# Kernel optimization log

Measured on AMD Instinct MI355X. Metric: run time of the kernel, lower is better.

Reference implementation:

```python
import jax, jax.numpy as jnp
import numpy as np

NUM_BINS = 4
NUM_CELLS = NUM_BINS ** 3


def _generate_grids(num_bins):
    # cell-center coordinates in the unit cube, matching generate_grids()
    c = (jnp.arange(num_bins, dtype=jnp.float32) + 1.0) / num_bins - 0.5 / num_bins
    gx, gy, gz = jnp.meshgrid(c, c, c, indexing='ij')
    return jnp.stack([gx.ravel(), gy.ravel(), gz.ravel()], axis=1)  # [C, 3]


def setup_inputs() -> dict:
    key = jax.random.key(0)
    x = jax.random.normal(key, (64, 65536, 6), dtype=jnp.float32)
    return {"input": x}


def reference(input):
    B, P, _ = input.shape
    pos = input[..., 0:3]
    ori = input[..., 3:6]

    # symmetric bounding cube: bbox_max over points and xyz dims
    bbox_max = jnp.max(jnp.abs(pos), axis=(1, 2), keepdims=True)          # [B,1,1]
    thickness = jnp.clip(2.0 * bbox_max, 1e-5, None)
    pos_in_cube = (pos + bbox_max) / thickness                            # [B,P,3] in [0,1]

    ci = jnp.clip((pos_in_cube * NUM_BINS).astype(jnp.int32), 0, NUM_BINS - 1)
    cell_idx = (ci[..., 0] * NUM_BINS + ci[..., 1]) * NUM_BINS + ci[..., 2]  # [B,P]

    seg = lambda vals, idx: jax.ops.segment_sum(vals, idx, num_segments=NUM_CELLS)

    # per-cell point counts
    freq = jax.vmap(seg)(jnp.ones((B, P), jnp.float32), cell_idx)[..., None]  # [B,C,1]
    freq_c = jnp.clip(freq, 1.0, None)
    uprefix = 1.0 / jnp.sqrt(freq_c)
    f_freq = 0.001 * freq * uprefix                                       # [B,C,1]

    # mean offset from cell centers
    grids = _generate_grids(NUM_BINS)                                     # [C,3]
    offsets = pos_in_cube - grids[cell_idx]                               # [B,P,3]
    f_mean = jax.vmap(seg)(offsets, cell_idx) * uprefix                   # [B,C,3]

    # upper-triangular orientation covariance: xx,xy,xz,yy,yz,zz
    ox, oy, oz = ori[..., 0], ori[..., 1], ori[..., 2]
    cov = jnp.stack([ox * ox, ox * oy, ox * oz, oy * oy, oy * oz, oz * oz], axis=-1)  # [B,P,6]
    f_normcov = jax.vmap(seg)(cov, cell_idx) / freq_c                     # [B,C,6]

    f_all = jnp.concatenate([f_freq, f_mean, f_normcov], axis=2).reshape(B, -1)  # [B, C*10]
    norm = jnp.linalg.norm(f_all, axis=1, keepdims=True)
    return f_all / jnp.clip(norm, 1e-12, None)
```

## Files before the change

kernel.cpp:

```cpp
#include <hip/hip_runtime.h>


#define BATCH 64
#define NPTS 65536
#define FEAT 640
#define COPIES 16
#define CSTRIDE 16
#define S_OFF 262144.0f
#define S_COV 4096.0f

__device__ __forceinline__ void bin_point(int* h, int k,
                                          float px, float py, float pz,
                                          float ox, float oy, float oz,
                                          float bmax, float inv_thick) {
    float sx = (px + bmax) * inv_thick;
    float sy = (py + bmax) * inv_thick;
    float sz = (pz + bmax) * inv_thick;
    int cx = (int)(sx * 4.0f); cx = cx < 0 ? 0 : (cx > 3 ? 3 : cx);
    int cy = (int)(sy * 4.0f); cy = cy < 0 ? 0 : (cy > 3 ? 3 : cy);
    int cz = (int)(sz * 4.0f); cz = cz < 0 ? 0 : (cz > 3 ? 3 : cz);
    int cell = (cx * 4 + cy) * 4 + cz;
    float offx = sx - (cx * 0.25f + 0.125f);
    float offy = sy - (cy * 0.25f + 0.125f);
    float offz = sz - (cz * 0.25f + 0.125f);
    int kk = k ^ (cell & 15);
    int a = cell * (10 * CSTRIDE) + kk;
    atomicAdd(&h[a + 0 * CSTRIDE], 1);
    atomicAdd(&h[a + 1 * CSTRIDE], __float2int_rn(offx * S_OFF));
    atomicAdd(&h[a + 2 * CSTRIDE], __float2int_rn(offy * S_OFF));
    atomicAdd(&h[a + 3 * CSTRIDE], __float2int_rn(offz * S_OFF));
    atomicAdd(&h[a + 4 * CSTRIDE], __float2int_rn(ox * ox * S_COV));
    atomicAdd(&h[a + 5 * CSTRIDE], __float2int_rn(ox * oy * S_COV));
    atomicAdd(&h[a + 6 * CSTRIDE], __float2int_rn(ox * oz * S_COV));
    atomicAdd(&h[a + 7 * CSTRIDE], __float2int_rn(oy * oy * S_COV));
    atomicAdd(&h[a + 8 * CSTRIDE], __float2int_rn(oy * oz * S_COV));
    atomicAdd(&h[a + 9 * CSTRIDE], __float2int_rn(oz * oz * S_COV));
}

__global__ __launch_bounds__(256) void k_bbox(const float* __restrict__ x,
                                              unsigned int* __restrict__ part,
                                              unsigned long long* __restrict__ acc) {
    int b = blockIdx.y;
    int fb = b * 16 + blockIdx.x;
    if (threadIdx.x < 40) acc[fb * 40 + threadIdx.x] = 0ULL;

    const float4* F = (const float4*)(x + (size_t)b * NPTS * 6);
    int tid = blockIdx.x * 256 + threadIdx.x;
    int tm = tid % 3;
    float m = 0.0f;
    #pragma unroll
    for (int o = 0; o < 2; ++o) {
        #pragma unroll
        for (int u = 0; u < 12; ++u) {
            int it = o * 12 + u;
            float4 v = F[tid + it * 4096];
            int mm = tm + (u % 3);
            mm = mm >= 3 ? mm - 3 : mm;
            float ax = fabsf(v.x), ay = fabsf(v.y), az = fabsf(v.z), aw = fabsf(v.w);
            float c0 = fmaxf(fmaxf(ax, ay), az);
            float c1 = fmaxf(az, aw);
            float cand = mm == 0 ? c0 : (mm == 1 ? c1 : ax);
            m = fmaxf(m, cand);
        }
    }
    for (int off = 32; off > 0; off >>= 1) m = fmaxf(m, __shfl_down(m, off, 64));
    __shared__ float s[4];
    if ((threadIdx.x & 63) == 0) s[threadIdx.x >> 6] = m;
    __syncthreads();
    if (threadIdx.x == 0) {
        m = fmaxf(fmaxf(s[0], s[1]), fmaxf(s[2], s[3]));
        part[fb] = __float_as_uint(m);
    }
}

__global__ __launch_bounds__(256) void k_bin(const float* __restrict__ x,
                                             const unsigned int* __restrict__ part,
                                             unsigned long long* __restrict__ acc) {
    __shared__ int h[FEAT * CSTRIDE];
    for (int i = threadIdx.x; i < FEAT * CSTRIDE; i += 256) h[i] = 0;
    int b = blockIdx.y;
    unsigned int um = 0u;
    #pragma unroll
    for (int p = 0; p < 16; ++p) um = um > part[b * 16 + p] ? um : part[b * 16 + p];
    float bmax = __uint_as_float(um);
    float thick = fmaxf(2.0f * bmax, 1e-5f);
    float inv_thick = 1.0f / thick;
    __syncthreads();

    const float4* base = (const float4*)(x + (size_t)b * NPTS * 6);
    int tid = blockIdx.x * 256 + threadIdx.x;
    int k = threadIdx.x & (COPIES - 1);
    #pragma unroll
    for (int it = 0; it < 8; ++it) {
        int i = tid + it * 4096;
        float4 f0 = base[3 * i + 0];
        float4 f1 = base[3 * i + 1];
        float4 f2 = base[3 * i + 2];
        bin_point(h, k, f0.x, f0.y, f0.z, f0.w, f1.x, f1.y, bmax, inv_thick);
        bin_point(h, k, f1.z, f1.w, f2.x, f2.y, f2.z, f2.w, bmax, inv_thick);
    }
    __syncthreads();
    for (int v = threadIdx.x; v < FEAT; v += 256) {
        long long sum = 0;
        #pragma unroll
        for (int c = 0; c < COPIES; ++c) sum += (long long)h[v * CSTRIDE + c];
        atomicAdd(&acc[b * FEAT + v], (unsigned long long)sum);
    }
}

__global__ __launch_bounds__(640) void k_final(const unsigned long long* __restrict__ acc,
                                               float* __restrict__ out) {
    int b = blockIdx.x;
    int t = threadIdx.x;
    int cell = t / 10, j = t - cell * 10;
    long long ni = (long long)acc[b * FEAT + cell * 10];
    long long vi = (long long)acc[b * FEAT + t];
    float n = (float)ni;
    float fc = fmaxf(n, 1.0f);
    float up = 1.0f / sqrtf(fc);
    float val;
    if (j == 0)      val = 0.001f * n * up;
    else if (j < 4)  val = ((float)vi * (1.0f / S_OFF)) * up;
    else             val = ((float)vi * (1.0f / S_COV)) / fc;

    __shared__ float red[12];
    float s = val * val;
    for (int off = 32; off > 0; off >>= 1) s += __shfl_down(s, off, 64);
    if ((t & 63) == 0) red[t >> 6] = s;
    __syncthreads();
    if (t == 0) {
        float tot = 0.0f;
        #pragma unroll
        for (int w = 0; w < 10; ++w) tot += red[w];
        red[10] = fmaxf(sqrtf(tot), 1e-12f);
    }
    __syncthreads();
    out[b * FEAT + t] = val / red[10];
}

extern "C" void kernel_launch(void* const* d_in, const int* in_sizes, int n_in,
                              void* d_out, int out_size, void* d_ws, size_t ws_size,
                              hipStream_t stream) {
    const float* x = (const float*)d_in[0];
    float* out = (float*)d_out;
    unsigned int* part = (unsigned int*)d_ws;
    unsigned long long* acc = (unsigned long long*)((char*)d_ws + 4096);

    dim3 grid(16, BATCH);
    k_bbox<<<grid, 256, 0, stream>>>(x, part, acc);
    k_bin<<<grid, 256, 0, stream>>>(x, part, acc);
    k_final<<<BATCH, 640, 0, stream>>>(acc, out);
}
```

Measured before the change: 161.8 us.

## Fuse bbox and binning into one cooperative kernel with grid sync

Merges the bounding-box reduction and histogram binning into a single cooperative kernel. Each thread holds its points in registers across a grid-wide sync, so the input is read from memory only once instead of twice. It falls back to the two-kernel path if the cooperative launch fails. The trade-offs are a grid barrier, the requirement that all blocks be resident, and higher register pressure from 24 float4 values per thread.

```diff
diff --git a/kernel.cpp b/kernel.cpp
--- a/kernel.cpp
+++ b/kernel.cpp
@@ -1,4 +1,7 @@
 #include <hip/hip_runtime.h>
+#include <hip/hip_cooperative_groups.h>
+
+namespace cg = cooperative_groups;
 
 
 #define BATCH 64
@@ -37,6 +40,70 @@
     atomicAdd(&h[a + 9 * CSTRIDE], __float2int_rn(oz * oz * S_COV));
 }
 
+__global__ __launch_bounds__(256, 4)
+void k_fused(const float* __restrict__ x,
+             unsigned int* __restrict__ part,
+             unsigned long long* __restrict__ acc) {
+    __shared__ int h[FEAT * CSTRIDE];
+    int b = blockIdx.y;
+    int fb = b * 16 + blockIdx.x;
+    int t = threadIdx.x;
+
+    const float4* base = (const float4*)(x + (size_t)b * NPTS * 6);
+    int tid = blockIdx.x * 256 + t;
+    float4 d[24];
+    #pragma unroll
+    for (int it = 0; it < 8; ++it) {
+        int i = tid + it * 4096;
+        d[it * 3 + 0] = base[3 * i + 0];
+        d[it * 3 + 1] = base[3 * i + 1];
+        d[it * 3 + 2] = base[3 * i + 2];
+    }
+    if (t < 40) acc[fb * 40 + t] = 0ULL;
+
+    float m = 0.0f;
+    #pragma unroll
+    for (int it = 0; it < 8; ++it) {
+        float4 f0 = d[it * 3 + 0], f1 = d[it * 3 + 1], f2 = d[it * 3 + 2];
+        m = fmaxf(m, fabsf(f0.x)); m = fmaxf(m, fabsf(f0.y)); m = fmaxf(m, fabsf(f0.z));
+        m = fmaxf(m, fabsf(f1.z)); m = fmaxf(m, fabsf(f1.w)); m = fmaxf(m, fabsf(f2.x));
+    }
+    for (int off = 32; off > 0; off >>= 1) m = fmaxf(m, __shfl_down(m, off, 64));
+    if ((t & 63) == 0) h[t >> 6] = __float_as_int(m);
+    __syncthreads();
+    if (t == 0) {
+        float bm = fmaxf(fmaxf(__int_as_float(h[0]), __int_as_float(h[1])),
+                         fmaxf(__int_as_float(h[2]), __int_as_float(h[3])));
+        part[fb] = __float_as_uint(bm);
+    }
+    __syncthreads();
+    for (int i = t; i < FEAT * CSTRIDE; i += 256) h[i] = 0;
+
+    cg::this_grid().sync();
+
+    unsigned int um = 0u;
+    #pragma unroll
+    for (int p = 0; p < 16; ++p) um = um > part[b * 16 + p] ? um : part[b * 16 + p];
+    float bmax = __uint_as_float(um);
+    float thick = fmaxf(2.0f * bmax, 1e-5f);
+    float inv_thick = 1.0f / thick;
+
+    int k = t & (COPIES - 1);
+    #pragma unroll
+    for (int it = 0; it < 8; ++it) {
+        float4 f0 = d[it * 3 + 0], f1 = d[it * 3 + 1], f2 = d[it * 3 + 2];
+        bin_point(h, k, f0.x, f0.y, f0.z, f0.w, f1.x, f1.y, bmax, inv_thick);
+        bin_point(h, k, f1.z, f1.w, f2.x, f2.y, f2.z, f2.w, bmax, inv_thick);
+    }
+    __syncthreads();
+    for (int v = t; v < FEAT; v += 256) {
+        long long sum = 0;
+        #pragma unroll
+        for (int c = 0; c < COPIES; ++c) sum += (long long)h[v * CSTRIDE + c];
+        atomicAdd(&acc[b * FEAT + v], (unsigned long long)sum);
+    }
+}
+
 __global__ __launch_bounds__(256) void k_bbox(const float* __restrict__ x,
                                               unsigned int* __restrict__ part,
                                               unsigned long long* __restrict__ acc) {
@@ -146,8 +213,14 @@
     unsigned int* part = (unsigned int*)d_ws;
     unsigned long long* acc = (unsigned long long*)((char*)d_ws + 4096);
 
-    dim3 grid(16, BATCH);
-    k_bbox<<<grid, 256, 0, stream>>>(x, part, acc);
-    k_bin<<<grid, 256, 0, stream>>>(x, part, acc);
+    void* args[] = { (void*)&x, (void*)&part, (void*)&acc };
+    hipError_t err = hipLaunchCooperativeKernel((void*)k_fused,
+                                                dim3(16, BATCH), dim3(256),
+                                                args, 0, stream);
+    if (err != hipSuccess) {
+        dim3 grid(16, BATCH);
+        k_bbox<<<grid, 256, 0, stream>>>(x, part, acc);
+        k_bin<<<grid, 256, 0, stream>>>(x, part, acc);
+    }
     k_final<<<BATCH, 640, 0, stream>>>(acc, out);
 }
```

Result: slower. 273.5 us (+69.1%).
